# Performance work log

Measured on AMD Instinct MI355X. Metric: run time of the kernel, lower is better.

The kernel has to match this reference:

```python
import jax, jax.numpy as jnp
import numpy as np

DIM = 128          # observed dim
LATENT = 128       # SDE state_size
HID = 128          # mu hidden width (hard-coded in source)
BROWNIAN = 2       # brownian_size
N_STEPS = 200      # Euler-Maruyama steps over t in [0, 1]
DT = 1.0 / N_STEPS


def _linear_init(key, fan_in, fan_out):
    # torch nn.Linear default: U(-1/sqrt(fan_in), 1/sqrt(fan_in))
    kw, kb = jax.random.split(key)
    bound = 1.0 / np.sqrt(fan_in)
    w = jax.random.uniform(kw, (fan_in, fan_out), jnp.float32, -bound, bound)
    b = jax.random.uniform(kb, (fan_out,), jnp.float32, -bound, bound)
    return w, b


def setup_inputs() -> dict:
    key = jax.random.key(0)
    ks = jax.random.split(key, 8)
    y = jax.random.normal(ks[0], (32768, DIM), jnp.float32)
    noise = jax.random.normal(ks[1], (N_STEPS, 32768, BROWNIAN), jnp.float32)
    enc_w, enc_b = _linear_init(ks[2], DIM, LATENT)
    mu_w1, mu_b1 = _linear_init(ks[3], LATENT, HID)
    mu_w2, mu_b2 = _linear_init(ks[4], HID, LATENT)
    sig_w, sig_b = _linear_init(ks[5], LATENT, LATENT * BROWNIAN)
    dec_w, dec_b = _linear_init(ks[6], LATENT, DIM)
    return {
        "y": y, "noise": noise,
        "enc_w": enc_w, "enc_b": enc_b,
        "mu_w1": mu_w1, "mu_b1": mu_b1, "mu_w2": mu_w2, "mu_b2": mu_b2,
        "sig_w": sig_w, "sig_b": sig_b,
        "dec_w": dec_w, "dec_b": dec_b,
    }


def reference(y, noise, enc_w, enc_b, mu_w1, mu_b1, mu_w2, mu_b2, sig_w, sig_b, dec_w, dec_b):
    B = y.shape[0]
    # encoder: Linear + exact GELU (torch nn.GELU default)
    z0 = jax.nn.gelu(y @ enc_w + enc_b, approximate=False)

    sqrt_dt = jnp.asarray(np.sqrt(DT), jnp.float32)

    def drift(z):  # f(t, y) = mu(y)
        h = jax.nn.gelu(z @ mu_w1 + mu_b1, approximate=False)
        return h @ mu_w2 + mu_b2

    def diffusion(z):  # g(t, y) -> [B, state, brownian]
        return (z @ sig_w + sig_b).reshape(B, LATENT, BROWNIAN)

    def step(z, xi):
        # Euler-Maruyama (Ito): z += f*dt + g @ dW,  dW = sqrt(dt)*xi
        dW = xi * sqrt_dt                      # [B, K]
        g = diffusion(z)                       # [B, D, K]
        z = z + drift(z) * DT + jnp.einsum("bdk,bk->bd", g, dW)
        return z, None

    zT, _ = jax.lax.scan(step, z0, noise)
    return zT @ dec_w + dec_b
```

## Files before the change

kernel.cpp:

```cpp
#include <hip/hip_runtime.h>
#include <math.h>

#define NSTEPS 200
#define NT     512
#define BR     64
#define SQDT_F 0.07071067811865475f
#define DT_F   0.005f
#define LOSCL  4096.0f
#define LOINV  2.44140625e-4f

typedef float  f32x4 __attribute__((ext_vector_type(4)));
typedef short  s16x8 __attribute__((ext_vector_type(8)));
typedef _Float16 h16x8 __attribute__((ext_vector_type(8)));
typedef unsigned short u16;
typedef unsigned short us4 __attribute__((ext_vector_type(4)));

#define ENC_OFF 0
#define W1_OFF  32768
#define W2_OFF  65536
#define WG0_OFF 98304
#define WG1_OFF 131072
#define DEC_OFF 163840
#define WPK_TOT 196608

__device__ __forceinline__ u16 f2h(float v) {
    _Float16 h = (_Float16)v;
    return __builtin_bit_cast(u16, h);
}
__device__ __forceinline__ float h2f(u16 u) {
    return (float)__builtin_bit_cast(_Float16, u);
}
__device__ __forceinline__ u16 split_hi(float v) { return f2h(v); }
__device__ __forceinline__ u16 split_lo(float v, u16 hi) {
    return f2h((v - h2f(hi)) * LOSCL);
}
__device__ __forceinline__ float gelu_exact(float x) {
    return 0.5f * x * (1.0f + erff(x * 0.70710678118654752f));
}

__device__ __forceinline__ void mfma16(f32x4& d, s16x8 a, s16x8 b) {
    d = __builtin_amdgcn_mfma_f32_16x16x32_f16(
            __builtin_bit_cast(h16x8, a), __builtin_bit_cast(h16x8, b), d, 0, 0, 0);
}
__device__ __forceinline__ s16x8 ldf(const u16* p) {
    return *reinterpret_cast<const s16x8*>(p);
}

__global__ void prepack(const float* __restrict__ enc_w, const float* __restrict__ mu_w1,
                        const float* __restrict__ mu_w2, const float* __restrict__ sig_w,
                        const float* __restrict__ dec_w, u16* __restrict__ wpk)
{
    int u = blockIdx.x * 256 + threadIdx.x;
    if (u >= WPK_TOT) return;
    int mat  = u >> 15;
    int r    = u & 32767;
    int i    = r & 7;
    int lane = (r >> 3) & 63;
    int term = (r >> 9) & 1;
    int kc   = (r >> 10) & 3;
    int nt   = (r >> 12) & 7;
    int k = kc * 32 + (lane >> 4) * 8 + i;
    int n = nt * 16 + (lane & 15);
    float v;
    switch (mat) {
        case 0:  v = enc_w[k * 128 + n];         break;
        case 1:  v = mu_w1[k * 128 + n];         break;
        case 2:  v = mu_w2[k * 128 + n];         break;
        case 3:  v = sig_w[k * 256 + 2 * n];     break;
        case 4:  v = sig_w[k * 256 + 2 * n + 1]; break;
        default: v = dec_w[k * 128 + n];         break;
    }
    u16 hi = split_hi(v);
    wpk[u] = term ? split_lo(v, hi) : hi;
}

__global__ __launch_bounds__(NT) void sde_mfma(
    const float* __restrict__ y, const float* __restrict__ noise,
    const float* __restrict__ enc_b, const float* __restrict__ mu_b1,
    const float* __restrict__ mu_b2, const float* __restrict__ sig_b,
    const float* __restrict__ dec_b, const u16* __restrict__ wpk,
    float* __restrict__ out, int Btot)
{
    __shared__ __align__(16) u16 zbh[8192];
    __shared__ __align__(16) u16 zbl[8192];
    __shared__ __align__(16) u16 hbh[8192];
    __shared__ __align__(16) u16 hbl[8192];
    __shared__ float nsb[2][128];

    const int tid  = threadIdx.x;
    const int lane = tid & 63, wid = tid >> 6;
    const int ln   = lane & 15, lg = lane >> 4;
    const size_t brow = (size_t)blockIdx.x * BR;

    const int n0 = wid * 16 + ln;
    const float b10 = mu_b1[n0];
    const float b20 = mu_b2[n0];
    const float bg0 = sig_b[2 * n0];
    const float bg1 = sig_b[2 * n0 + 1];

    #pragma unroll
    for (int c = 0; c < 4; c++) {
        int q = c * NT + tid;
        int row = q >> 5, k4 = (q & 31) << 2;
        const float4 v = *reinterpret_cast<const float4*>(y + (brow + row) * 128 + k4);
        int idx = row * 128 + ((((k4 >> 3) ^ (row & 7))) << 3) + (k4 & 7);
        float vv[4] = {v.x, v.y, v.z, v.w};
        us4 hv, lv;
        #pragma unroll
        for (int e = 0; e < 4; e++) {
            u16 h = split_hi(vv[e]);
            u16 l = split_lo(vv[e], h);
            hv[e] = h; lv[e] = l;
        }
        *reinterpret_cast<us4*>(zbh + idx) = hv;
        *reinterpret_cast<us4*>(zbl + idx) = lv;
    }
    __syncthreads();

    float z0v[4][4];
    {
        const float be0 = enc_b[n0];
        f32x4 a0[4], a1[4];
        #pragma unroll
        for (int mt = 0; mt < 4; mt++) {
            a0[mt] = f32x4{be0, be0, be0, be0};
            a1[mt] = f32x4{0, 0, 0, 0};
        }
        #pragma unroll
        for (int kc = 0; kc < 4; kc++) {
            int fo = (((wid << 2) | kc) << 10) + (lane << 3);
            s16x8 bh = ldf(wpk + ENC_OFF + fo);
            s16x8 bl = ldf(wpk + ENC_OFF + fo + 512);
            #pragma unroll
            for (int mt = 0; mt < 4; mt++) {
                int row = mt * 16 + ln;
                int idx = row * 128 + ((((kc << 2) | lg) ^ (row & 7)) << 3);
                s16x8 ah = ldf(zbh + idx);
                s16x8 al = ldf(zbl + idx);
                mfma16(a0[mt], ah, bh);
                mfma16(a1[mt], al, bh);
                mfma16(a1[mt], ah, bl);
            }
        }
        #pragma unroll
        for (int mt = 0; mt < 4; mt++)
            #pragma unroll
            for (int r = 0; r < 4; r++)
                z0v[mt][r] = gelu_exact(fmaf(a1[mt][r], LOINV, a0[mt][r]));
    }
    __syncthreads();

    #pragma unroll
    for (int mt = 0; mt < 4; mt++)
        #pragma unroll
        for (int r = 0; r < 4; r++) {
            int m = 16 * mt + 4 * lg + r;
            int idx = m * 128 + ((((n0 >> 3) ^ (m & 7))) << 3) + (n0 & 7);
            u16 h = split_hi(z0v[mt][r]);
            zbh[idx] = h;
            zbl[idx] = split_lo(z0v[mt][r], h);
        }
    if (tid < 128) nsb[0][tid] = noise[brow * 2 + tid];
    __syncthreads();

    const u16* wq = wpk;

    for (int t = 0; t < NSTEPS; t++) {
        asm volatile("" : "+s"(wq));
        {
            int tn = (t + 1 < NSTEPS) ? (t + 1) : t;
            if (tid < 128) nsb[(t + 1) & 1][tid] = noise[((size_t)tn * Btot + brow) * 2 + tid];
        }
        {
            f32x4 a0[4], a1[4];
            #pragma unroll
            for (int mt = 0; mt < 4; mt++) {
                a0[mt] = f32x4{b10, b10, b10, b10};
                a1[mt] = f32x4{0, 0, 0, 0};
            }
            #pragma unroll
            for (int kc = 0; kc < 4; kc++) {
                int fo = (((wid << 2) | kc) << 10) + (lane << 3);
                s16x8 bh = ldf(wq + W1_OFF + fo);
                s16x8 bl = ldf(wq + W1_OFF + fo + 512);
                #pragma unroll
                for (int mt = 0; mt < 4; mt++) {
                    int row = mt * 16 + ln;
                    int idx = row * 128 + ((((kc << 2) | lg) ^ (row & 7)) << 3);
                    s16x8 ah = ldf(zbh + idx);
                    s16x8 al = ldf(zbl + idx);
                    mfma16(a0[mt], ah, bh);
                    mfma16(a1[mt], al, bh);
                    mfma16(a1[mt], ah, bl);
                }
            }
            #pragma unroll
            for (int mt = 0; mt < 4; mt++)
                #pragma unroll
                for (int r = 0; r < 4; r++) {
                    float hv = gelu_exact(fmaf(a1[mt][r], LOINV, a0[mt][r]));
                    int m = 16 * mt + 4 * lg + r;
                    int idx = m * 128 + ((((n0 >> 3) ^ (m & 7))) << 3) + (n0 & 7);
                    u16 h = split_hi(hv);
                    hbh[idx] = h;
                    hbl[idx] = split_lo(hv, h);
                }
        }
        float sdelta[4][4];
        {
            f32x4 q0h[4], q0l[4], q1h[4], q1l[4];
            #pragma unroll
            for (int mt = 0; mt < 4; mt++) {
                q0h[mt] = f32x4{bg0, bg0, bg0, bg0}; q0l[mt] = f32x4{0, 0, 0, 0};
                q1h[mt] = f32x4{bg1, bg1, bg1, bg1}; q1l[mt] = f32x4{0, 0, 0, 0};
            }
            #pragma unroll 1
            for (int kc = 0; kc < 4; kc++) {
                int fo = (((wid << 2) | kc) << 10) + (lane << 3);
                s16x8 b0h = ldf(wq + WG0_OFF + fo);
                s16x8 b0l = ldf(wq + WG0_OFF + fo + 512);
                s16x8 b1h = ldf(wq + WG1_OFF + fo);
                s16x8 b1l = ldf(wq + WG1_OFF + fo + 512);
                #pragma unroll
                for (int mt = 0; mt < 4; mt++) {
                    int row = mt * 16 + ln;
                    int idx = row * 128 + ((((kc << 2) | lg) ^ (row & 7)) << 3);
                    s16x8 ah = ldf(zbh + idx);
                    s16x8 al = ldf(zbl + idx);
                    mfma16(q0h[mt], ah, b0h);
                    mfma16(q0l[mt], al, b0h);
                    mfma16(q0l[mt], ah, b0l);
                    mfma16(q1h[mt], ah, b1h);
                    mfma16(q1l[mt], al, b1h);
                    mfma16(q1l[mt], ah, b1l);
                }
            }
            const float* np = nsb[t & 1];
            #pragma unroll
            for (int mt = 0; mt < 4; mt++)
                #pragma unroll
                for (int r = 0; r < 4; r++) {
                    int m = 16 * mt + 4 * lg + r;
                    float dw0 = np[2 * m] * SQDT_F;
                    float dw1 = np[2 * m + 1] * SQDT_F;
                    float gv0 = fmaf(q0l[mt][r], LOINV, q0h[mt][r]);
                    float gv1 = fmaf(q1l[mt][r], LOINV, q1h[mt][r]);
                    sdelta[mt][r] = fmaf(gv0, dw0, gv1 * dw1);
                }
        }
        __syncthreads();

        {
            f32x4 a0[4], a1[4];
            #pragma unroll
            for (int mt = 0; mt < 4; mt++) {
                a0[mt] = f32x4{b20, b20, b20, b20};
                a1[mt] = f32x4{0, 0, 0, 0};
            }
            #pragma unroll
            for (int kc = 0; kc < 4; kc++) {
                int fo = (((wid << 2) | kc) << 10) + (lane << 3);
                s16x8 bh = ldf(wq + W2_OFF + fo);
                s16x8 bl = ldf(wq + W2_OFF + fo + 512);
                #pragma unroll
                for (int mt = 0; mt < 4; mt++) {
                    int row = mt * 16 + ln;
                    int idx = row * 128 + ((((kc << 2) | lg) ^ (row & 7)) << 3);
                    s16x8 ah = ldf(hbh + idx);
                    s16x8 al = ldf(hbl + idx);
                    mfma16(a0[mt], ah, bh);
                    mfma16(a1[mt], al, bh);
                    mfma16(a1[mt], ah, bl);
                }
            }
            #pragma unroll
            for (int mt = 0; mt < 4; mt++)
                #pragma unroll
                for (int r = 0; r < 4; r++) {
                    int m = 16 * mt + 4 * lg + r;
                    int idx = m * 128 + ((((n0 >> 3) ^ (m & 7))) << 3) + (n0 & 7);
                    float z = fmaf(h2f(zbl[idx]), LOINV, h2f(zbh[idx]));
                    float drift = fmaf(a1[mt][r], LOINV, a0[mt][r]);
                    float v = fmaf(drift, DT_F, z + sdelta[mt][r]);
                    u16 h = split_hi(v);
                    zbh[idx] = h;
                    zbl[idx] = split_lo(v, h);
                }
        }
        __syncthreads();
    }

    {
        const float bd0 = dec_b[n0];
        f32x4 a0[4], a1[4];
        #pragma unroll
        for (int mt = 0; mt < 4; mt++) {
            a0[mt] = f32x4{bd0, bd0, bd0, bd0};
            a1[mt] = f32x4{0, 0, 0, 0};
        }
        #pragma unroll
        for (int kc = 0; kc < 4; kc++) {
            int fo = (((wid << 2) | kc) << 10) + (lane << 3);
            s16x8 bh = ldf(wpk + DEC_OFF + fo);
            s16x8 bl = ldf(wpk + DEC_OFF + fo + 512);
            #pragma unroll
            for (int mt = 0; mt < 4; mt++) {
                int row = mt * 16 + ln;
                int idx = row * 128 + ((((kc << 2) | lg) ^ (row & 7)) << 3);
                s16x8 ah = ldf(zbh + idx);
                s16x8 al = ldf(zbl + idx);
                mfma16(a0[mt], ah, bh);
                mfma16(a1[mt], al, bh);
                mfma16(a1[mt], ah, bl);
            }
        }
        #pragma unroll
        for (int mt = 0; mt < 4; mt++)
            #pragma unroll
            for (int r = 0; r < 4; r++) {
                int m = 16 * mt + 4 * lg + r;
                out[(brow + m) * 128 + n0] = fmaf(a1[mt][r], LOINV, a0[mt][r]);
            }
    }
}

extern "C" void kernel_launch(void* const* d_in, const int* in_sizes, int n_in,
                              void* d_out, int out_size, void* d_ws, size_t ws_size,
                              hipStream_t stream) {
    const float* y     = (const float*)d_in[0];
    const float* noise = (const float*)d_in[1];
    const float* enc_w = (const float*)d_in[2];
    const float* enc_b = (const float*)d_in[3];
    const float* mu_w1 = (const float*)d_in[4];
    const float* mu_b1 = (const float*)d_in[5];
    const float* mu_w2 = (const float*)d_in[6];
    const float* mu_b2 = (const float*)d_in[7];
    const float* sig_w = (const float*)d_in[8];
    const float* sig_b = (const float*)d_in[9];
    const float* dec_w = (const float*)d_in[10];
    const float* dec_b = (const float*)d_in[11];
    float* out = (float*)d_out;
    u16* wpk = (u16*)d_ws;

    const int Btot = in_sizes[0] / 128;
    prepack<<<(WPK_TOT + 255) / 256, 256, 0, stream>>>(enc_w, mu_w1, mu_w2, sig_w, dec_w, wpk);
    sde_mfma<<<Btot / BR, NT, 0, stream>>>(y, noise, enc_b, mu_b1, mu_b2, sig_b, dec_b,
                                           wpk, out, Btot);
}
```

Measured before the change: 2.946 ms.

## Fuse mu-W1 and sigma GEMMs into one pass over z and refine LDS swizzle

Result: slower. 3.139 ms (+6.6%).

```diff
diff --git a/kernel.cpp b/kernel.cpp
--- a/kernel.cpp
+++ b/kernel.cpp
@@ -44,6 +44,10 @@
 }
 __device__ __forceinline__ s16x8 ldf(const u16* p) {
     return *reinterpret_cast<const s16x8*>(p);
+}
+
+__device__ __forceinline__ int swz(int row) {
+    return (row & 7) ^ ((row & 8) >> 2);
 }
 
 __global__ void prepack(const float* __restrict__ enc_w, const float* __restrict__ mu_w1,
@@ -97,13 +101,14 @@
     const float b20 = mu_b2[n0];
     const float bg0 = sig_b[2 * n0];
     const float bg1 = sig_b[2 * n0 + 1];
+    const int swzl = swz(ln);
 
     #pragma unroll
     for (int c = 0; c < 4; c++) {
         int q = c * NT + tid;
         int row = q >> 5, k4 = (q & 31) << 2;
         const float4 v = *reinterpret_cast<const float4*>(y + (brow + row) * 128 + k4);
-        int idx = row * 128 + ((((k4 >> 3) ^ (row & 7))) << 3) + (k4 & 7);
+        int idx = row * 128 + (((k4 >> 3) ^ swz(row)) << 3) + (k4 & 7);
         float vv[4] = {v.x, v.y, v.z, v.w};
         us4 hv, lv;
         #pragma unroll
@@ -133,8 +138,7 @@
             s16x8 bl = ldf(wpk + ENC_OFF + fo + 512);
             #pragma unroll
             for (int mt = 0; mt < 4; mt++) {
-                int row = mt * 16 + ln;
-                int idx = row * 128 + ((((kc << 2) | lg) ^ (row & 7)) << 3);
+                int idx = (mt * 16 + ln) * 128 + ((((kc << 2) | lg) ^ swzl) << 3);
                 s16x8 ah = ldf(zbh + idx);
                 s16x8 al = ldf(zbl + idx);
                 mfma16(a0[mt], ah, bh);
@@ -155,7 +159,7 @@
         #pragma unroll
         for (int r = 0; r < 4; r++) {
             int m = 16 * mt + 4 * lg + r;
-            int idx = m * 128 + ((((n0 >> 3) ^ (m & 7))) << 3) + (n0 & 7);
+            int idx = m * 128 + (((n0 >> 3) ^ swz(m)) << 3) + (n0 & 7);
             u16 h = split_hi(z0v[mt][r]);
             zbh[idx] = h;
             zbl[idx] = split_lo(z0v[mt][r], h);
@@ -171,82 +175,64 @@
             int tn = (t + 1 < NSTEPS) ? (t + 1) : t;
             if (tid < 128) nsb[(t + 1) & 1][tid] = noise[((size_t)tn * Btot + brow) * 2 + tid];
         }
-        {
-            f32x4 a0[4], a1[4];
-            #pragma unroll
-            for (int mt = 0; mt < 4; mt++) {
-                a0[mt] = f32x4{b10, b10, b10, b10};
-                a1[mt] = f32x4{0, 0, 0, 0};
-            }
-            #pragma unroll
+        float sdelta[4][4];
+        const float* np = nsb[t & 1];
+        #pragma unroll
+        for (int half = 0; half < 2; half++) {
+            f32x4 a0[2], a1[2], q0h[2], q0l[2], q1h[2], q1l[2];
+            #pragma unroll
+            for (int u = 0; u < 2; u++) {
+                a0[u]  = f32x4{b10, b10, b10, b10};  a1[u]  = f32x4{0, 0, 0, 0};
+                q0h[u] = f32x4{bg0, bg0, bg0, bg0};  q0l[u] = f32x4{0, 0, 0, 0};
+                q1h[u] = f32x4{bg1, bg1, bg1, bg1};  q1l[u] = f32x4{0, 0, 0, 0};
+            }
+            #pragma unroll 2
             for (int kc = 0; kc < 4; kc++) {
                 int fo = (((wid << 2) | kc) << 10) + (lane << 3);
-                s16x8 bh = ldf(wq + W1_OFF + fo);
-                s16x8 bl = ldf(wq + W1_OFF + fo + 512);
-                #pragma unroll
-                for (int mt = 0; mt < 4; mt++) {
-                    int row = mt * 16 + ln;
-                    int idx = row * 128 + ((((kc << 2) | lg) ^ (row & 7)) << 3);
+                s16x8 b1h = ldf(wq + W1_OFF  + fo);
+                s16x8 b1l = ldf(wq + W1_OFF  + fo + 512);
+                s16x8 c0h = ldf(wq + WG0_OFF + fo);
+                s16x8 c0l = ldf(wq + WG0_OFF + fo + 512);
+                s16x8 c1h = ldf(wq + WG1_OFF + fo);
+                s16x8 c1l = ldf(wq + WG1_OFF + fo + 512);
+                #pragma unroll
+                for (int u = 0; u < 2; u++) {
+                    int idx = ((half * 2 + u) * 16 + ln) * 128 + ((((kc << 2) | lg) ^ swzl) << 3);
                     s16x8 ah = ldf(zbh + idx);
                     s16x8 al = ldf(zbl + idx);
-                    mfma16(a0[mt], ah, bh);
-                    mfma16(a1[mt], al, bh);
-                    mfma16(a1[mt], ah, bl);
-                }
-            }
-            #pragma unroll
-            for (int mt = 0; mt < 4; mt++)
-                #pragma unroll
-                for (int r = 0; r < 4; r++) {
-                    float hv = gelu_exact(fmaf(a1[mt][r], LOINV, a0[mt][r]));
-                    int m = 16 * mt + 4 * lg + r;
-                    int idx = m * 128 + ((((n0 >> 3) ^ (m & 7))) << 3) + (n0 & 7);
-                    u16 h = split_hi(hv);
-                    hbh[idx] = h;
-                    hbl[idx] = split_lo(hv, h);
-                }
-        }
-        float sdelta[4][4];
-        {
-            f32x4 q0h[4], q0l[4], q1h[4], q1l[4];
-            #pragma unroll
-            for (int mt = 0; mt < 4; mt++) {
-                q0h[mt] = f32x4{bg0, bg0, bg0, bg0}; q0l[mt] = f32x4{0, 0, 0, 0};
-                q1h[mt] = f32x4{bg1, bg1, bg1, bg1}; q1l[mt] = f32x4{0, 0, 0, 0};
-            }
-            #pragma unroll 1
-            for (int kc = 0; kc < 4; kc++) {
-                int fo = (((wid << 2) | kc) << 10) + (lane << 3);
-                s16x8 b0h = ldf(wq + WG0_OFF + fo);
-                s16x8 b0l = ldf(wq + WG0_OFF + fo + 512);
-                s16x8 b1h = ldf(wq + WG1_OFF + fo);
-                s16x8 b1l = ldf(wq + WG1_OFF + fo + 512);
-                #pragma unroll
-                for (int mt = 0; mt < 4; mt++) {
-                    int row = mt * 16 + ln;
-                    int idx = row * 128 + ((((kc << 2) | lg) ^ (row & 7)) << 3);
-                    s16x8 ah = ldf(zbh + idx);
-                    s16x8 al = ldf(zbl + idx);
-                    mfma16(q0h[mt], ah, b0h);
-                    mfma16(q0l[mt], al, b0h);
-                    mfma16(q0l[mt], ah, b0l);
-                    mfma16(q1h[mt], ah, b1h);
-                    mfma16(q1l[mt], al, b1h);
-                    mfma16(q1l[mt], ah, b1l);
-                }
-            }
-            const float* np = nsb[t & 1];
-            #pragma unroll
-            for (int mt = 0; mt < 4; mt++)
+                    mfma16(a0[u],  ah, b1h);
+                    mfma16(a1[u],  al, b1h);
+                    mfma16(a1[u],  ah, b1l);
+                    mfma16(q0h[u], ah, c0h);
+                    mfma16(q0l[u], al, c0h);
+                    mfma16(q0l[u], ah, c0l);
+                    mfma16(q1h[u], ah, c1h);
+                    mfma16(q1l[u], al, c1h);
+                    mfma16(q1l[u], ah, c1l);
+                }
+            }
+            #pragma unroll
+            for (int u = 0; u < 2; u++) {
+                const int mt = half * 2 + u;
                 #pragma unroll
                 for (int r = 0; r < 4; r++) {
                     int m = 16 * mt + 4 * lg + r;
                     float dw0 = np[2 * m] * SQDT_F;
                     float dw1 = np[2 * m + 1] * SQDT_F;
-                    float gv0 = fmaf(q0l[mt][r], LOINV, q0h[mt][r]);
-                    float gv1 = fmaf(q1l[mt][r], LOINV, q1h[mt][r]);
+                    float gv0 = fmaf(q0l[u][r], LOINV, q0h[u][r]);
+                    float gv1 = fmaf(q1l[u][r], LOINV, q1h[u][r]);
                     sdelta[mt][r] = fmaf(gv0, dw0, gv1 * dw1);
                 }
+                #pragma unroll
+                for (int r = 0; r < 4; r++) {
+                    float hv = gelu_exact(fmaf(a1[u][r], LOINV, a0[u][r]));
+                    int m = 16 * mt + 4 * lg + r;
+                    int idx = m * 128 + (((n0 >> 3) ^ swz(m)) << 3) + (n0 & 7);
+                    u16 h = split_hi(hv);
+                    hbh[idx] = h;
+                    hbl[idx] = split_lo(hv, h);
+                }
+            }
         }
         __syncthreads();
 
@@ -264,8 +250,7 @@
                 s16x8 bl = ldf(wq + W2_OFF + fo + 512);
                 #pragma unroll
                 for (int mt = 0; mt < 4; mt++) {
-                    int row = mt * 16 + ln;
-                    int idx = row * 128 + ((((kc << 2) | lg) ^ (row & 7)) << 3);
+                    int idx = (mt * 16 + ln) * 128 + ((((kc << 2) | lg) ^ swzl) << 3);
                     s16x8 ah = ldf(hbh + idx);
                     s16x8 al = ldf(hbl + idx);
                     mfma16(a0[mt], ah, bh);
@@ -278,7 +263,7 @@
                 #pragma unroll
                 for (int r = 0; r < 4; r++) {
                     int m = 16 * mt + 4 * lg + r;
-                    int idx = m * 128 + ((((n0 >> 3) ^ (m & 7))) << 3) + (n0 & 7);
+                    int idx = m * 128 + (((n0 >> 3) ^ swz(m)) << 3) + (n0 & 7);
                     float z = fmaf(h2f(zbl[idx]), LOINV, h2f(zbh[idx]));
                     float drift = fmaf(a1[mt][r], LOINV, a0[mt][r]);
                     float v = fmaf(drift, DT_F, z + sdelta[mt][r]);
@@ -305,8 +290,7 @@
             s16x8 bl = ldf(wpk + DEC_OFF + fo + 512);
             #pragma unroll
             for (int mt = 0; mt < 4; mt++) {
-                int row = mt * 16 + ln;
-                int idx = row * 128 + ((((kc << 2) | lg) ^ (row & 7)) << 3);
+                int idx = (mt * 16 + ln) * 128 + ((((kc << 2) | lg) ^ swzl) << 3);
                 s16x8 ah = ldf(zbh + idx);
                 s16x8 al = ldf(zbl + idx);
                 mfma16(a0[mt], ah, bh);
```
